# Kernel optimization log

Hardware: AMD Instinct MI355X
Metric: run time of the kernel (lower is better)

## Reference

```python
import jax, jax.numpy as jnp
import numpy as np

DIM = 96
K = 3
STRIDE = 1
PAD = 1
RED = 4
BN_EPS = 1e-5


def setup_inputs() -> dict:
    key = jax.random.key(0)
    ks = jax.random.split(key, 8)
    b, c, h, w = 32, DIM, 128, 128
    cr = DIM // RED
    return {
        "x": jax.random.normal(ks[0], (b, c, h, w), jnp.float32),
        "w1": jax.random.normal(ks[1], (cr, c), jnp.float32) * 0.1,          # conv1 1x1, no bias
        "gamma": jnp.ones((cr,), jnp.float32),
        "beta": jnp.zeros((cr,), jnp.float32),
        "running_mean": jax.random.normal(ks[2], (cr,), jnp.float32) * 0.1,
        "running_var": jax.random.uniform(ks[3], (cr,), jnp.float32, 0.5, 1.5),
        "w2": jax.random.normal(ks[4], (DIM * K * K, cr), jnp.float32) * 0.1,  # conv2 1x1
        "b2": jax.random.normal(ks[5], (DIM * K * K,), jnp.float32) * 0.1,
        "bias": jnp.zeros((DIM,), jnp.float32),
    }


def _dynamic_weight(x, w1, gamma, beta, running_mean, running_var, w2, b2):
    # AdaptiveAvgPool2d((1,1)) -> [b, c]
    pooled = jnp.mean(x, axis=(2, 3))
    # conv1 (1x1, no bias) on 1x1 spatial == matmul
    h1 = pooled @ w1.T  # [b, c//r]
    # BatchNorm2d in inference mode (running stats)
    h1 = (h1 - running_mean) * jax.lax.rsqrt(running_var + BN_EPS) * gamma + beta
    h1 = jax.nn.sigmoid(h1)
    # conv2 (1x1) == matmul + bias -> [b, dim*k*k]
    wdyn = h1 @ w2.T + b2
    return wdyn.reshape(x.shape[0], DIM, K, K)


def _per_sample_depthwise(x, weight, bias):
    # x: [b, c, h, w], weight: [b, c, k, k] -> per-sample depthwise conv
    def one(xi, wi):
        # xi: [c,h,w], wi: [c,k,k]
        out = jax.lax.conv_general_dilated(
            xi[None], wi[:, None],
            window_strides=(STRIDE, STRIDE),
            padding=[(PAD, PAD), (PAD, PAD)],
            dimension_numbers=("NCHW", "OIHW", "NCHW"),
            feature_group_count=DIM,
        )
        return out[0]

    y = jax.vmap(one)(x, weight)  # [b, c, h', w']
    return y + bias[None, :, None, None]


def reference(x, w1, gamma, beta, running_mean, running_var, w2, b2, bias):
    weight = _dynamic_weight(x, w1, gamma, beta, running_mean, running_var, w2, b2)
    return _per_sample_depthwise(x, weight, bias)
```

## Files before the change

kernel.cpp:

```cpp
#include <hip/hip_runtime.h>
#include <math.h>

#define C_DIM 96
#define CR 24
#define H_DIM 128
#define W_DIM 128
#define B_DIM 32
#define CHUNKS 4
#define ROWS_PER_CHUNK (H_DIM / CHUNKS)

typedef float nfloat4 __attribute__((ext_vector_type(4)));

__global__ void pool_kernel(const float* __restrict__ x, float* __restrict__ pooled) {
    int plane = blockIdx.x;
    const float4* xp = (const float4*)(x + (size_t)plane * (H_DIM * W_DIM));
    float s = 0.f;
    for (int i = threadIdx.x; i < 4096; i += 256) {
        float4 v = xp[i];
        s += v.x + v.y + v.z + v.w;
    }
    for (int off = 32; off; off >>= 1) s += __shfl_down(s, off, 64);
    __shared__ float ls[4];
    int lane = threadIdx.x & 63, wv = threadIdx.x >> 6;
    if (lane == 0) ls[wv] = s;
    __syncthreads();
    if (threadIdx.x == 0) {
        float t = ls[0] + ls[1] + ls[2] + ls[3];
        pooled[plane] = t * (1.f / (H_DIM * W_DIM));
    }
}

__global__ void __launch_bounds__(256) fused_dwconv_kernel(const float* __restrict__ x,
                                                           const float* __restrict__ pooled,
                                                           const float* __restrict__ w1,
                                                           const float* __restrict__ gamma,
                                                           const float* __restrict__ beta,
                                                           const float* __restrict__ rmean,
                                                           const float* __restrict__ rvar,
                                                           const float* __restrict__ w2,
                                                           const float* __restrict__ b2,
                                                           const float* __restrict__ bias,
                                                           float* __restrict__ out) {
    int tid = threadIdx.x;
    int plane0 = blockIdx.x * 2;
    int b = plane0 / C_DIM;
    int c0 = plane0 % C_DIM;

    __shared__ float pl[C_DIM];
    __shared__ float h1[CR];
    __shared__ float wsm[2][10];

    if (tid < C_DIM) pl[tid] = pooled[b * C_DIM + tid];
    __syncthreads();
    if (tid < CR) {
        float s = 0.f;
        const float* wr = w1 + tid * C_DIM;
        #pragma unroll 8
        for (int c = 0; c < C_DIM; c++) s += pl[c] * wr[c];
        s = (s - rmean[tid]) * rsqrtf(rvar[tid] + 1e-5f) * gamma[tid] + beta[tid];
        h1[tid] = 1.f / (1.f + expf(-s));
    }
    __syncthreads();
    if (tid < 20) {
        if (tid < 18) {
            int p = tid / 9, k = tid % 9;
            int row = (c0 + p) * 9 + k;
            float s = b2[row];
            const float* wr = w2 + row * CR;
            #pragma unroll
            for (int j = 0; j < CR; j++) s += h1[j] * wr[j];
            wsm[p][k] = s;
        } else {
            wsm[tid - 18][9] = bias[c0 + (tid - 18)];
        }
    }
    __syncthreads();

    int g = tid & 31;
    int chunk = (tid >> 5) & 3;
    int p = tid >> 7;
    int plane = plane0 + p;
    int col = g << 2;
    int r0 = chunk * ROWS_PER_CHUNK;

    const float* xp = x + (size_t)plane * (H_DIM * W_DIM);
    float* op = out + (size_t)plane * (H_DIM * W_DIM);
    const float* wv = wsm[p];
    float w00 = wv[0], w01 = wv[1], w02 = wv[2];
    float w10 = wv[3], w11 = wv[4], w12 = wv[5];
    float w20 = wv[6], w21 = wv[7], w22 = wv[8];
    float bb = wv[9];
    const bool leftEdge = (g == 0), rightEdge = (g == 31);

    float4 pv, cv, nv;
    float plh, prh, clh, crh, nlh, nrh;

    {
        int r = r0 - 1;
        float4 v;
        if (r >= 0) v = *(const float4*)(xp + r * W_DIM + col);
        else { v.x = v.y = v.z = v.w = 0.f; }
        float l = __shfl_up(v.w, 1, 64);
        float rr = __shfl_down(v.x, 1, 64);
        pv = v; plh = leftEdge ? 0.f : l; prh = rightEdge ? 0.f : rr;
    }
    {
        float4 v = *(const float4*)(xp + r0 * W_DIM + col);
        float l = __shfl_up(v.w, 1, 64);
        float rr = __shfl_down(v.x, 1, 64);
        cv = v; clh = leftEdge ? 0.f : l; crh = rightEdge ? 0.f : rr;
    }

    #pragma unroll 4
    for (int i = 0; i < ROWS_PER_CHUNK; i++) {
        int r = r0 + i;
        float4 v;
        if (r + 1 < H_DIM) v = *(const float4*)(xp + (r + 1) * W_DIM + col);
        else { v.x = v.y = v.z = v.w = 0.f; }
        float l = __shfl_up(v.w, 1, 64);
        float rr = __shfl_down(v.x, 1, 64);
        nv = v; nlh = leftEdge ? 0.f : l; nrh = rightEdge ? 0.f : rr;

        nfloat4 o;
        o.x = w00 * plh  + w01 * pv.x + w02 * pv.y
            + w10 * clh  + w11 * cv.x + w12 * cv.y
            + w20 * nlh  + w21 * nv.x + w22 * nv.y + bb;
        o.y = w00 * pv.x + w01 * pv.y + w02 * pv.z
            + w10 * cv.x + w11 * cv.y + w12 * cv.z
            + w20 * nv.x + w21 * nv.y + w22 * nv.z + bb;
        o.z = w00 * pv.y + w01 * pv.z + w02 * pv.w
            + w10 * cv.y + w11 * cv.z + w12 * cv.w
            + w20 * nv.y + w21 * nv.z + w22 * nv.w + bb;
        o.w = w00 * pv.z + w01 * pv.w + w02 * prh
            + w10 * cv.z + w11 * cv.w + w12 * crh
            + w20 * nv.z + w21 * nv.w + w22 * nrh + bb;
        __builtin_nontemporal_store(o, (nfloat4*)(op + r * W_DIM + col));

        pv = cv; plh = clh; prh = crh;
        cv = nv; clh = nlh; crh = nrh;
    }
}

extern "C" void kernel_launch(void* const* d_in, const int* in_sizes, int n_in,
                              void* d_out, int out_size, void* d_ws, size_t ws_size,
                              hipStream_t stream) {
    const float* x     = (const float*)d_in[0];
    const float* w1    = (const float*)d_in[1];
    const float* gamma = (const float*)d_in[2];
    const float* beta  = (const float*)d_in[3];
    const float* rmean = (const float*)d_in[4];
    const float* rvar  = (const float*)d_in[5];
    const float* w2    = (const float*)d_in[6];
    const float* b2    = (const float*)d_in[7];
    const float* bias  = (const float*)d_in[8];
    float* out = (float*)d_out;

    float* pooled = (float*)d_ws;

    pool_kernel<<<B_DIM * C_DIM, 256, 0, stream>>>(x, pooled);
    fused_dwconv_kernel<<<B_DIM * C_DIM / 2, 256, 0, stream>>>(
        x, pooled, w1, gamma, beta, rmean, rvar, w2, b2, bias, out);
}
```

Baseline: 387.6 us.

## Fuse pooling and dynamic depthwise conv into one persistent work-queue kernel

The separate pooling and conv kernels are merged into one persistent kernel with 2048 blocks. Blocks first pull pooling tasks from an atomic counter, publishing each plane mean and bumping a per-batch completion counter. They then pull conv tasks and spin-wait until all 96 channel means of the sample are ready. This lets conv work for early batches overlap pooling of later ones and removes a kernel boundary. The cost is a memset launch, atomic contention, spin-waits, and reliance on every launched block being resident to avoid deadlock.

```diff
diff --git a/kernel.cpp b/kernel.cpp
--- a/kernel.cpp
+++ b/kernel.cpp
@@ -6,138 +6,166 @@
 #define H_DIM 128
 #define W_DIM 128
 #define B_DIM 32
-#define CHUNKS 4
-#define ROWS_PER_CHUNK (H_DIM / CHUNKS)
+#define N_PLANES (B_DIM * C_DIM)
+#define N_CONV   (N_PLANES / 2)
+#define GRID 2048
+#define ROWS_PER_CHUNK 32
 
 typedef float nfloat4 __attribute__((ext_vector_type(4)));
 
-__global__ void pool_kernel(const float* __restrict__ x, float* __restrict__ pooled) {
-    int plane = blockIdx.x;
-    const float4* xp = (const float4*)(x + (size_t)plane * (H_DIM * W_DIM));
-    float s = 0.f;
-    for (int i = threadIdx.x; i < 4096; i += 256) {
-        float4 v = xp[i];
-        s += v.x + v.y + v.z + v.w;
+
+__global__ void __launch_bounds__(256) fused_all_kernel(const float* __restrict__ x,
+                                                        const float* __restrict__ w1,
+                                                        const float* __restrict__ gamma,
+                                                        const float* __restrict__ beta,
+                                                        const float* __restrict__ rmean,
+                                                        const float* __restrict__ rvar,
+                                                        const float* __restrict__ w2,
+                                                        const float* __restrict__ b2,
+                                                        const float* __restrict__ bias,
+                                                        float* __restrict__ out,
+                                                        int* __restrict__ ctrl,
+                                                        float* __restrict__ pooled) {
+    int tid = threadIdx.x;
+    __shared__ int task;
+    __shared__ float red[4];
+
+    for (;;) {
+        if (tid == 0) task = atomicAdd(&ctrl[0], 1);
+        __syncthreads();
+        int t = task;
+        __syncthreads();
+        if (t >= N_PLANES) break;
+
+        const float4* xp = (const float4*)(x + (size_t)t * (H_DIM * W_DIM));
+        float s = 0.f;
+        for (int i = tid; i < 4096; i += 256) {
+            float4 v = xp[i];
+            s += v.x + v.y + v.z + v.w;
+        }
+        for (int off = 32; off; off >>= 1) s += __shfl_down(s, off, 64);
+        if ((tid & 63) == 0) red[tid >> 6] = s;
+        __syncthreads();
+        if (tid == 0) {
+            float m = (red[0] + red[1] + red[2] + red[3]) * (1.f / (H_DIM * W_DIM));
+            __hip_atomic_store(&pooled[t], m, __ATOMIC_RELAXED, __HIP_MEMORY_SCOPE_AGENT);
+            __hip_atomic_fetch_add(&ctrl[2 + t / C_DIM], 1, __ATOMIC_RELEASE, __HIP_MEMORY_SCOPE_AGENT);
+        }
+        __syncthreads();
     }
-    for (int off = 32; off; off >>= 1) s += __shfl_down(s, off, 64);
-    __shared__ float ls[4];
-    int lane = threadIdx.x & 63, wv = threadIdx.x >> 6;
-    if (lane == 0) ls[wv] = s;
-    __syncthreads();
-    if (threadIdx.x == 0) {
-        float t = ls[0] + ls[1] + ls[2] + ls[3];
-        pooled[plane] = t * (1.f / (H_DIM * W_DIM));
-    }
-}
-
-__global__ void __launch_bounds__(256) fused_dwconv_kernel(const float* __restrict__ x,
-                                                           const float* __restrict__ pooled,
-                                                           const float* __restrict__ w1,
-                                                           const float* __restrict__ gamma,
-                                                           const float* __restrict__ beta,
-                                                           const float* __restrict__ rmean,
-                                                           const float* __restrict__ rvar,
-                                                           const float* __restrict__ w2,
-                                                           const float* __restrict__ b2,
-                                                           const float* __restrict__ bias,
-                                                           float* __restrict__ out) {
-    int tid = threadIdx.x;
-    int plane0 = blockIdx.x * 2;
-    int b = plane0 / C_DIM;
-    int c0 = plane0 % C_DIM;
 
     __shared__ float pl[C_DIM];
     __shared__ float h1[CR];
     __shared__ float wsm[2][10];
 
-    if (tid < C_DIM) pl[tid] = pooled[b * C_DIM + tid];
-    __syncthreads();
-    if (tid < CR) {
-        float s = 0.f;
-        const float* wr = w1 + tid * C_DIM;
-        #pragma unroll 8
-        for (int c = 0; c < C_DIM; c++) s += pl[c] * wr[c];
-        s = (s - rmean[tid]) * rsqrtf(rvar[tid] + 1e-5f) * gamma[tid] + beta[tid];
-        h1[tid] = 1.f / (1.f + expf(-s));
-    }
-    __syncthreads();
-    if (tid < 20) {
-        if (tid < 18) {
-            int p = tid / 9, k = tid % 9;
-            int row = (c0 + p) * 9 + k;
-            float s = b2[row];
-            const float* wr = w2 + row * CR;
-            #pragma unroll
-            for (int j = 0; j < CR; j++) s += h1[j] * wr[j];
-            wsm[p][k] = s;
-        } else {
-            wsm[tid - 18][9] = bias[c0 + (tid - 18)];
+    for (;;) {
+        if (tid == 0) task = atomicAdd(&ctrl[1], 1);
+        __syncthreads();
+        int t = task;
+        __syncthreads();
+        if (t >= N_CONV) return;
+
+        int plane0 = t * 2;
+        int b = plane0 / C_DIM;
+        int c0 = plane0 % C_DIM;
+
+        if (tid == 0) {
+            while (__hip_atomic_load(&ctrl[2 + b], __ATOMIC_ACQUIRE, __HIP_MEMORY_SCOPE_AGENT) < C_DIM)
+                __builtin_amdgcn_s_sleep(8);
         }
-    }
-    __syncthreads();
+        __syncthreads();
 
-    int g = tid & 31;
-    int chunk = (tid >> 5) & 3;
-    int p = tid >> 7;
-    int plane = plane0 + p;
-    int col = g << 2;
-    int r0 = chunk * ROWS_PER_CHUNK;
+        if (tid < C_DIM)
+            pl[tid] = __hip_atomic_load(&pooled[b * C_DIM + tid], __ATOMIC_RELAXED, __HIP_MEMORY_SCOPE_AGENT);
+        __syncthreads();
+        if (tid < CR) {
+            float s = 0.f;
+            const float* wr = w1 + tid * C_DIM;
+            #pragma unroll 8
+            for (int c = 0; c < C_DIM; c++) s += pl[c] * wr[c];
+            s = (s - rmean[tid]) * rsqrtf(rvar[tid] + 1e-5f) * gamma[tid] + beta[tid];
+            h1[tid] = 1.f / (1.f + expf(-s));
+        }
+        __syncthreads();
+        if (tid < 20) {
+            if (tid < 18) {
+                int p = tid / 9, k = tid % 9;
+                int row = (c0 + p) * 9 + k;
+                float s = b2[row];
+                const float* wr = w2 + row * CR;
+                #pragma unroll
+                for (int j = 0; j < CR; j++) s += h1[j] * wr[j];
+                wsm[p][k] = s;
+            } else {
+                wsm[tid - 18][9] = bias[c0 + (tid - 18)];
+            }
+        }
+        __syncthreads();
 
-    const float* xp = x + (size_t)plane * (H_DIM * W_DIM);
-    float* op = out + (size_t)plane * (H_DIM * W_DIM);
-    const float* wv = wsm[p];
-    float w00 = wv[0], w01 = wv[1], w02 = wv[2];
-    float w10 = wv[3], w11 = wv[4], w12 = wv[5];
-    float w20 = wv[6], w21 = wv[7], w22 = wv[8];
-    float bb = wv[9];
-    const bool leftEdge = (g == 0), rightEdge = (g == 31);
+        int g = tid & 31;
+        int chunk = (tid >> 5) & 3;
+        int p = tid >> 7;
+        int plane = plane0 + p;
+        int col = g << 2;
+        int r0 = chunk * ROWS_PER_CHUNK;
 
-    float4 pv, cv, nv;
-    float plh, prh, clh, crh, nlh, nrh;
+        const float* xp = x + (size_t)plane * (H_DIM * W_DIM);
+        float* op = out + (size_t)plane * (H_DIM * W_DIM);
+        const float* wv = wsm[p];
+        float w00 = wv[0], w01 = wv[1], w02 = wv[2];
+        float w10 = wv[3], w11 = wv[4], w12 = wv[5];
+        float w20 = wv[6], w21 = wv[7], w22 = wv[8];
+        float bb = wv[9];
+        const bool leftEdge = (g == 0), rightEdge = (g == 31);
 
-    {
-        int r = r0 - 1;
-        float4 v;
-        if (r >= 0) v = *(const float4*)(xp + r * W_DIM + col);
-        else { v.x = v.y = v.z = v.w = 0.f; }
-        float l = __shfl_up(v.w, 1, 64);
-        float rr = __shfl_down(v.x, 1, 64);
-        pv = v; plh = leftEdge ? 0.f : l; prh = rightEdge ? 0.f : rr;
-    }
-    {
-        float4 v = *(const float4*)(xp + r0 * W_DIM + col);
-        float l = __shfl_up(v.w, 1, 64);
-        float rr = __shfl_down(v.x, 1, 64);
-        cv = v; clh = leftEdge ? 0.f : l; crh = rightEdge ? 0.f : rr;
-    }
+        float4 pv, cv, nv;
+        float plh, prh, clh, crh, nlh, nrh;
 
-    #pragma unroll 4
-    for (int i = 0; i < ROWS_PER_CHUNK; i++) {
-        int r = r0 + i;
-        float4 v;
-        if (r + 1 < H_DIM) v = *(const float4*)(xp + (r + 1) * W_DIM + col);
-        else { v.x = v.y = v.z = v.w = 0.f; }
-        float l = __shfl_up(v.w, 1, 64);
-        float rr = __shfl_down(v.x, 1, 64);
-        nv = v; nlh = leftEdge ? 0.f : l; nrh = rightEdge ? 0.f : rr;
+        {
+            int r = r0 - 1;
+            float4 v;
+            if (r >= 0) v = *(const float4*)(xp + r * W_DIM + col);
+            else { v.x = v.y = v.z = v.w = 0.f; }
+            float l = __shfl_up(v.w, 1, 64);
+            float rr = __shfl_down(v.x, 1, 64);
+            pv = v; plh = leftEdge ? 0.f : l; prh = rightEdge ? 0.f : rr;
+        }
+        {
+            float4 v = *(const float4*)(xp + r0 * W_DIM + col);
+            float l = __shfl_up(v.w, 1, 64);
+            float rr = __shfl_down(v.x, 1, 64);
+            cv = v; clh = leftEdge ? 0.f : l; crh = rightEdge ? 0.f : rr;
+        }
 
-        nfloat4 o;
-        o.x = w00 * plh  + w01 * pv.x + w02 * pv.y
-            + w10 * clh  + w11 * cv.x + w12 * cv.y
-            + w20 * nlh  + w21 * nv.x + w22 * nv.y + bb;
-        o.y = w00 * pv.x + w01 * pv.y + w02 * pv.z
-            + w10 * cv.x + w11 * cv.y + w12 * cv.z
-            + w20 * nv.x + w21 * nv.y + w22 * nv.z + bb;
-        o.z = w00 * pv.y + w01 * pv.z + w02 * pv.w
-            + w10 * cv.y + w11 * cv.z + w12 * cv.w
-            + w20 * nv.y + w21 * nv.z + w22 * nv.w + bb;
-        o.w = w00 * pv.z + w01 * pv.w + w02 * prh
-            + w10 * cv.z + w11 * cv.w + w12 * crh
-            + w20 * nv.z + w21 * nv.w + w22 * nrh + bb;
-        __builtin_nontemporal_store(o, (nfloat4*)(op + r * W_DIM + col));
+        #pragma unroll 4
+        for (int i = 0; i < ROWS_PER_CHUNK; i++) {
+            int r = r0 + i;
+            float4 v;
+            if (r + 1 < H_DIM) v = *(const float4*)(xp + (r + 1) * W_DIM + col);
+            else { v.x = v.y = v.z = v.w = 0.f; }
+            float l = __shfl_up(v.w, 1, 64);
+            float rr = __shfl_down(v.x, 1, 64);
+            nv = v; nlh = leftEdge ? 0.f : l; nrh = rightEdge ? 0.f : rr;
 
-        pv = cv; plh = clh; prh = crh;
-        cv = nv; clh = nlh; crh = nrh;
+            nfloat4 o;
+            o.x = w00 * plh  + w01 * pv.x + w02 * pv.y
+                + w10 * clh  + w11 * cv.x + w12 * cv.y
+                + w20 * nlh  + w21 * nv.x + w22 * nv.y + bb;
+            o.y = w00 * pv.x + w01 * pv.y + w02 * pv.z
+                + w10 * cv.x + w11 * cv.y + w12 * cv.z
+                + w20 * nv.x + w21 * nv.y + w22 * nv.z + bb;
+            o.z = w00 * pv.y + w01 * pv.z + w02 * pv.w
+                + w10 * cv.y + w11 * cv.z + w12 * cv.w
+                + w20 * nv.y + w21 * nv.z + w22 * nv.w + bb;
+            o.w = w00 * pv.z + w01 * pv.w + w02 * prh
+                + w10 * cv.z + w11 * cv.w + w12 * crh
+                + w20 * nv.z + w21 * nv.w + w22 * nrh + bb;
+            __builtin_nontemporal_store(o, (nfloat4*)(op + r * W_DIM + col));
+
+            pv = cv; plh = clh; prh = crh;
+            cv = nv; clh = nlh; crh = nrh;
+        }
+        __syncthreads();
     }
 }
 
@@ -155,9 +183,10 @@
     const float* bias  = (const float*)d_in[8];
     float* out = (float*)d_out;
 
-    float* pooled = (float*)d_ws;
+    int*   ctrl   = (int*)d_ws;
+    float* pooled = (float*)((char*)d_ws + 256);
 
-    pool_kernel<<<B_DIM * C_DIM, 256, 0, stream>>>(x, pooled);
-    fused_dwconv_kernel<<<B_DIM * C_DIM / 2, 256, 0, stream>>>(
-        x, pooled, w1, gamma, beta, rmean, rvar, w2, b2, bias, out);
+    hipMemsetAsync(d_ws, 0, 256, stream);
+    fused_all_kernel<<<GRID, 256, 0, stream>>>(
+        x, w1, gamma, beta, rmean, rvar, w2, b2, bias, out, ctrl, pooled);
 }
```

Result: slower. 546.4 us (+41.0%).
